# Optimization experiments

Measured on AMD Instinct MI355X. Metric: run time of the kernel, lower is better.

The kernel has to match this reference:

```python
import jax, jax.numpy as jnp
import numpy as np

EMBED_DIM = 768
NUM_HEADS = 12
HEAD_DIM = EMBED_DIM // NUM_HEADS
B, N = 4, 2048


def setup_inputs() -> dict:
    key = jax.random.key(0)
    k_x, k_wqkv, k_bqkv, k_wo, k_bo = jax.random.split(key, 5)
    s = 1.0 / np.sqrt(EMBED_DIM)
    return {
        "x": jax.random.normal(k_x, (B, N, EMBED_DIM), dtype=jnp.float32),
        # torch nn.Linear weight layout: [out_features, in_features]
        "w_qkv": jax.random.uniform(k_wqkv, (3 * EMBED_DIM, EMBED_DIM), minval=-s, maxval=s, dtype=jnp.float32),
        "b_qkv": jax.random.uniform(k_bqkv, (3 * EMBED_DIM,), minval=-s, maxval=s, dtype=jnp.float32),
        "w_out": jax.random.uniform(k_wo, (EMBED_DIM, EMBED_DIM), minval=-s, maxval=s, dtype=jnp.float32),
        "b_out": jax.random.uniform(k_bo, (EMBED_DIM,), minval=-s, maxval=s, dtype=jnp.float32),
    }


def reference(x, w_qkv, b_qkv, w_out, b_out):
    Bsz, Nlen, C = x.shape
    # fused QKV projection: [B, N, 3C]
    qkv = jnp.einsum("bnc,oc->bno", x, w_qkv) + b_qkv
    qkv = qkv.reshape(Bsz, Nlen, 3, NUM_HEADS, HEAD_DIM)
    q = qkv[:, :, 0].transpose(0, 2, 1, 3)  # [B, H, N, D]
    k = qkv[:, :, 1].transpose(0, 2, 1, 3)
    v = qkv[:, :, 2].transpose(0, 2, 1, 3)
    scale = 1.0 / np.sqrt(HEAD_DIM).astype(np.float32)
    scores = jnp.einsum("bhqd,bhkd->bhqk", q, k) * scale  # [B, H, N, N]
    attn = jax.nn.softmax(scores, axis=-1)
    ctx = jnp.einsum("bhqk,bhkd->bhqd", attn, v)  # [B, H, N, D]
    ctx = ctx.transpose(0, 2, 1, 3).reshape(Bsz, Nlen, C)
    return jnp.einsum("bnc,oc->bno", ctx, w_out) + b_out
```

## Files before the change

### kernel.cpp

```cpp
#include <hip/hip_runtime.h>
#include <math.h>

typedef __attribute__((ext_vector_type(8))) short bf16x8;
typedef __attribute__((ext_vector_type(4))) float f32x4;
typedef unsigned short u16;

namespace {
constexpr int BATCH = 4, SEQ = 2048, CDIM = 768, NH = 12, HD = 64;
constexpr int MROWS = BATCH * SEQ;
constexpr int KD = CDIM;
constexpr float QSCALE = 0.125f * 1.44269504088896f;
}

__device__ __forceinline__ u16 f2bf(float f) {
  unsigned x = __float_as_uint(f);
  return (u16)((x + 0x7fffu + ((x >> 16) & 1u)) >> 16);
}

__device__ __forceinline__ unsigned pk2bf(float a, float b) {
  unsigned r;
  asm("v_cvt_pk_bf16_f32 %0, %1, %2" : "=v"(r) : "v"(a), "v"(b));
  return r;
}

#if defined(__has_builtin)
#if __has_builtin(__builtin_amdgcn_exp2f)
#define EXP2(x) __builtin_amdgcn_exp2f(x)
#endif
#endif
#ifndef EXP2
#define EXP2(x) exp2f(x)
#endif

#define GLD16(gp, lp)                                                        \
  __builtin_amdgcn_global_load_lds(                                          \
      (const __attribute__((address_space(1))) void*)(gp),                   \
      (__attribute__((address_space(3))) void*)(lp), 16, 0, 0)

__global__ void convert_bf16(const float* __restrict__ x, u16* __restrict__ xb, int nx4,
                             const float* __restrict__ w1, u16* __restrict__ w1b, int n14,
                             const float* __restrict__ w2, u16* __restrict__ w2b, int n24) {
  const int stride = gridDim.x * blockDim.x;
  const int t0 = blockIdx.x * blockDim.x + threadIdx.x;
  for (int i = t0; i < nx4; i += stride) {
    float4 v = ((const float4*)x)[i];
    ushort4 o; o.x = f2bf(v.x); o.y = f2bf(v.y); o.z = f2bf(v.z); o.w = f2bf(v.w);
    ((ushort4*)xb)[i] = o;
  }
  for (int i = t0; i < n14; i += stride) {
    float4 v = ((const float4*)w1)[i];
    ushort4 o; o.x = f2bf(v.x); o.y = f2bf(v.y); o.z = f2bf(v.z); o.w = f2bf(v.w);
    ((ushort4*)w1b)[i] = o;
  }
  for (int i = t0; i < n24; i += stride) {
    float4 v = ((const float4*)w2)[i];
    ushort4 o; o.x = f2bf(v.x); o.y = f2bf(v.y); o.z = f2bf(v.z); o.w = f2bf(v.w);
    ((ushort4*)w2b)[i] = o;
  }
}

template <int MODE>
__global__ __launch_bounds__(512, 4) void gemm_bf16(
    const u16* __restrict__ A, const u16* __restrict__ Bw,
    const float* __restrict__ bias, float* __restrict__ outf,
    u16* __restrict__ qws, u16* __restrict__ kws, u16* __restrict__ vws) {
  __shared__ u16 smem[2 * 2 * 128 * 64];
  const int t = threadIdx.x;
  const int w = t >> 6, l = t & 63, g = l >> 4, li = l & 15;
  const int wm = w >> 1, wn = w & 1;
  const int lin = blockIdx.x;
  const int rowb = ((lin & 7) << 3) | ((lin >> 3) & 7);
  const int colb = lin >> 6;
  const int row0 = rowb * 128, col0 = colb * 128;

  const int srow = w * 16 + (l >> 3);
  const int skc = (l & 7) ^ (l >> 3);
  const u16* gA = A + (size_t)(row0 + srow) * KD + skc * 8;
  const u16* gB = Bw + (size_t)(col0 + srow) * KD + skc * 8;

  f32x4 acc[2][4];
#pragma unroll
  for (int a = 0; a < 2; ++a)
#pragma unroll
    for (int c = 0; c < 4; ++c) acc[a][c] = {0.f, 0.f, 0.f, 0.f};

#define GSTAGE(kt_, buf_)                                                     \
  do {                                                                        \
    const int k0_ = (kt_) * 64;                                               \
    u16* As_ = smem + (buf_) * (2 * 128 * 64);                                \
    u16* Bs_ = As_ + 128 * 64;                                                \
    _Pragma("unroll")                                                         \
    for (int j = 0; j < 2; ++j) {                                             \
      GLD16(gA + (size_t)8 * j * KD + k0_, &As_[(w * 16 + 8 * j) * 64]);      \
      GLD16(gB + (size_t)8 * j * KD + k0_, &Bs_[(w * 16 + 8 * j) * 64]);      \
    }                                                                         \
  } while (0)

  constexpr int NK = KD / 64;
  GSTAGE(0, 0);
  GSTAGE(1, 1);
  asm volatile("s_waitcnt vmcnt(4)" ::: "memory");
  __builtin_amdgcn_sched_barrier(0);
  __builtin_amdgcn_s_barrier();
  __builtin_amdgcn_sched_barrier(0);

  for (int kt = 0; kt < NK; ++kt) {
    const int cur = kt & 1;
    const u16* AsC = smem + cur * (2 * 128 * 64);
    const u16* BsC = AsC + 128 * 64;

    bf16x8 af[2][2], bfr[4][2];
#pragma unroll
    for (int mi = 0; mi < 2; ++mi) {
      const int r = wm * 32 + mi * 16 + li;
#pragma unroll
      for (int ks = 0; ks < 2; ++ks)
        af[mi][ks] = *(const bf16x8*)&AsC[r * 64 + (((ks * 4 + g) ^ (li & 7)) * 8)];
    }
#pragma unroll
    for (int ni = 0; ni < 4; ++ni) {
      const int r = wn * 64 + ni * 16 + li;
#pragma unroll
      for (int ks = 0; ks < 2; ++ks)
        bfr[ni][ks] = *(const bf16x8*)&BsC[r * 64 + (((ks * 4 + g) ^ (li & 7)) * 8)];
    }
    __builtin_amdgcn_s_setprio(1);
#pragma unroll
    for (int ni = 0; ni < 4; ++ni)
#pragma unroll
      for (int mi = 0; mi < 2; ++mi) {
        acc[mi][ni] = __builtin_amdgcn_mfma_f32_16x16x32_bf16(af[mi][0], bfr[ni][0], acc[mi][ni], 0, 0, 0);
        acc[mi][ni] = __builtin_amdgcn_mfma_f32_16x16x32_bf16(af[mi][1], bfr[ni][1], acc[mi][ni], 0, 0, 0);
      }
    __builtin_amdgcn_s_setprio(0);

    if (kt + 1 < NK) {
      asm volatile("s_waitcnt vmcnt(0)" ::: "memory");
      __builtin_amdgcn_sched_barrier(0);
      __builtin_amdgcn_s_barrier();
      __builtin_amdgcn_sched_barrier(0);
      if (kt + 2 < NK) GSTAGE(kt + 2, cur);
    }
  }
#undef GSTAGE

  float bsr[4];
#pragma unroll
  for (int ni = 0; ni < 4; ++ni) bsr[ni] = bias[col0 + wn * 64 + ni * 16 + li];
  const int bidx = row0 >> 11;
  const int nseq0 = row0 & (SEQ - 1);

  __syncthreads();

  if (MODE == 1) {
    float* Cf = (float*)smem;
#pragma unroll
    for (int p = 0; p < 4; ++p) {
      if (wm == p) {
#pragma unroll
        for (int mi = 0; mi < 2; ++mi)
#pragma unroll
          for (int ni = 0; ni < 4; ++ni)
#pragma unroll
            for (int i = 0; i < 4; ++i)
              Cf[(mi * 16 + 4 * g + i) * 132 + wn * 64 + ni * 16 + li] =
                  acc[mi][ni][i] + bsr[ni];
      }
      __syncthreads();
#pragma unroll
      for (int j = 0; j < 2; ++j) {
        const int fid = t + 512 * j;
        const int r = fid >> 5, c4 = (fid & 31) * 4;
        *(float4*)(outf + (size_t)(row0 + p * 32 + r) * CDIM + col0 + c4) =
            *(const float4*)&Cf[r * 132 + c4];
      }
      __syncthreads();
    }
  } else {
#pragma unroll
    for (int hc = 0; hc < 2; ++hc) {
      const int nb = col0 + hc * 64;
      const int s = nb / CDIM;
      const int h = (nb % CDIM) / HD;
      if (wn == hc) {
        if (s < 2) {
          const float qs = (s == 0) ? QSCALE : 1.f;
#pragma unroll
          for (int mi = 0; mi < 2; ++mi)
#pragma unroll
            for (int ni = 0; ni < 4; ++ni)
#pragma unroll
              for (int i = 0; i < 4; ++i)
                smem[(wm * 32 + mi * 16 + 4 * g + i) * 72 + ni * 16 + li] =
                    f2bf((acc[mi][ni][i] + bsr[ni]) * qs);
        } else {
#pragma unroll
          for (int mi = 0; mi < 2; ++mi)
#pragma unroll
            for (int ni = 0; ni < 4; ++ni)
#pragma unroll
              for (int i = 0; i < 4; ++i)
                smem[(ni * 16 + li) * 136 + wm * 32 + mi * 16 + 4 * g + i] =
                    f2bf(acc[mi][ni][i] + bsr[ni]);
        }
      }
      __syncthreads();
      if (s < 2) {
        u16* dst = (s == 0 ? qws : kws) + ((size_t)(bidx * NH + h) * SEQ + nseq0) * HD;
        const int r = t >> 3, c = (t & 7) * 8;
#pragma unroll
        for (int rd = 0; rd < 2; ++rd)
          *(uint4*)(dst + (size_t)(r + 64 * rd) * HD + c) =
              *(const uint4*)&smem[(r + 64 * rd) * 72 + c];
      } else {
        u16* dst = vws + (size_t)(bidx * NH + h) * HD * SEQ + nseq0;
        const int d = t >> 4, c = (t & 15) * 8;
#pragma unroll
        for (int rd = 0; rd < 2; ++rd)
          *(uint4*)(dst + (size_t)(d + 32 * rd) * SEQ + c) =
              *(const uint4*)&smem[(d + 32 * rd) * 136 + c];
      }
      __syncthreads();
    }
  }
}

__global__ __launch_bounds__(256, 3) void attn_mfma(
    const u16* __restrict__ qws, const u16* __restrict__ kws,
    const u16* __restrict__ vws, u16* __restrict__ ctx) {
  __shared__ u16 Ks[2][64 * 64];
  __shared__ u16 Vs[2][64 * 64];
  __shared__ u16 Ps[4 * 32 * 72];
  const int t = threadIdx.x;
  const int w = t >> 6, l = t & 63, g = l >> 4, li = l & 15;
  const int n = blockIdx.x;
  const int xcd = n & 7, j = n >> 3;
  const int hb = xcd * 6 + (j >> 4);
  const int q0 = (j & 15) * 128;
  const int h = hb % NH, b = hb / NH;
  const size_t bh = (size_t)b * NH + h;
  const u16* qb = qws + bh * SEQ * HD;
  const u16* kb = kws + bh * SEQ * HD;
  const u16* vb = vws + bh * HD * SEQ;

  bf16x8 qf[2][2];
#pragma unroll
  for (int qt = 0; qt < 2; ++qt)
#pragma unroll
    for (int ks = 0; ks < 2; ++ks)
      qf[qt][ks] = *(const bf16x8*)(qb + (size_t)(q0 + w * 32 + qt * 16 + li) * HD + ks * 32 + g * 8);
  asm volatile("s_waitcnt vmcnt(0)" ::: "memory");
  __builtin_amdgcn_sched_barrier(0);

  f32x4 acc[4][2];
#pragma unroll
  for (int dt = 0; dt < 4; ++dt)
#pragma unroll
    for (int qt = 0; qt < 2; ++qt) acc[dt][qt] = {0.f, 0.f, 0.f, 0.f};
  float lrun[2] = {0.f, 0.f};

  const int srow8 = l >> 3;
  const int skc = (l & 7) ^ srow8;
  const u16* gK = kb + (size_t)(w * 16 + srow8) * HD + skc * 8;
  const u16* gV = vb + (size_t)(w * 16 + srow8) * SEQ + skc * 8;
  u16* Pw = Ps + w * 32 * 72;

  constexpr int NT = SEQ / 64;

#define STAGE(kt_, buf_)                                                          \
  do {                                                                            \
    const int key0_ = (kt_) * 64;                                                 \
    GLD16(gK + (size_t)(key0_ + 0) * HD, &Ks[buf_][(w * 16 + 0) * 64]);           \
    GLD16(gV + (size_t)0 * SEQ + key0_, &Vs[buf_][(w * 16 + 0) * 64]);            \
    GLD16(gK + (size_t)(key0_ + 8) * HD, &Ks[buf_][(w * 16 + 8) * 64]);           \
    GLD16(gV + (size_t)8 * SEQ + key0_, &Vs[buf_][(w * 16 + 8) * 64]);            \
  } while (0)

  STAGE(0, 0);
  STAGE(1, 1);
  asm volatile("s_waitcnt vmcnt(4)" ::: "memory");
  __builtin_amdgcn_sched_barrier(0);
  __builtin_amdgcn_s_barrier();
  __builtin_amdgcn_sched_barrier(0);

  const f32x4 Z = {0.f, 0.f, 0.f, 0.f};

  for (int kt = 0; kt < NT; ++kt) {
    const int cur = kt & 1;
    const u16* KsC = Ks[cur];
    const u16* VsC = Vs[cur];

    f32x4 S[4][2];
    __builtin_amdgcn_s_setprio(1);
#pragma unroll
    for (int kb4 = 0; kb4 < 4; ++kb4) {
      bf16x8 kf0 = *(const bf16x8*)&KsC[(kb4 * 16 + li) * 64 + ((g ^ (li & 7)) * 8)];
      bf16x8 kf1 = *(const bf16x8*)&KsC[(kb4 * 16 + li) * 64 + (((4 + g) ^ (li & 7)) * 8)];
#pragma unroll
      for (int qt = 0; qt < 2; ++qt) {
        S[kb4][qt] = __builtin_amdgcn_mfma_f32_16x16x32_bf16(kf0, qf[qt][0], Z, 0, 0, 0);
        S[kb4][qt] = __builtin_amdgcn_mfma_f32_16x16x32_bf16(kf1, qf[qt][1], S[kb4][qt], 0, 0, 0);
      }
    }
    __builtin_amdgcn_s_setprio(0);

#pragma unroll
    for (int qt = 0; qt < 2; ++qt) {
      float rs = 0.f;
#pragma unroll
      for (int kb4 = 0; kb4 < 4; ++kb4) {
        const float p0 = EXP2(S[kb4][qt][0]);
        const float p1 = EXP2(S[kb4][qt][1]);
        const float p2 = EXP2(S[kb4][qt][2]);
        const float p3 = EXP2(S[kb4][qt][3]);
        rs += (p0 + p1) + (p2 + p3);
        uint2 pk;
        pk.x = pk2bf(p0, p1);
        pk.y = pk2bf(p2, p3);
        *(uint2*)&Pw[(qt * 16 + li) * 72 + ((kb4 ^ (li & 3)) * 16) + 4 * g] = pk;
      }
      lrun[qt] += rs;
    }

    bf16x8 vf[4][2];
#pragma unroll
    for (int dt = 0; dt < 4; ++dt) {
      vf[dt][0] = *(const bf16x8*)&VsC[(dt * 16 + li) * 64 + ((g ^ (li & 7)) * 8)];
      vf[dt][1] = *(const bf16x8*)&VsC[(dt * 16 + li) * 64 + (((4 + g) ^ (li & 7)) * 8)];
    }
    bf16x8 pf[2][2];
#pragma unroll
    for (int qt = 0; qt < 2; ++qt)
#pragma unroll
      for (int ks = 0; ks < 2; ++ks) {
        const int slot = (ks * 2 + (g >> 1)) ^ (li & 3);
        pf[qt][ks] = *(const bf16x8*)&Pw[(qt * 16 + li) * 72 + slot * 16 + (g & 1) * 8];
      }

    __builtin_amdgcn_s_setprio(1);
#pragma unroll
    for (int dt = 0; dt < 4; ++dt)
#pragma unroll
      for (int qt = 0; qt < 2; ++qt) {
        acc[dt][qt] = __builtin_amdgcn_mfma_f32_16x16x32_bf16(vf[dt][0], pf[qt][0], acc[dt][qt], 0, 0, 0);
        acc[dt][qt] = __builtin_amdgcn_mfma_f32_16x16x32_bf16(vf[dt][1], pf[qt][1], acc[dt][qt], 0, 0, 0);
      }
    __builtin_amdgcn_s_setprio(0);

    if (kt + 1 < NT) {
      asm volatile("s_waitcnt vmcnt(0)" ::: "memory");
      __builtin_amdgcn_sched_barrier(0);
      __builtin_amdgcn_s_barrier();
      __builtin_amdgcn_sched_barrier(0);
      if (kt + 2 < NT) STAGE(kt + 2, cur);
    }
  }
#undef STAGE

#pragma unroll
  for (int qt = 0; qt < 2; ++qt) {
    lrun[qt] += __shfl_xor(lrun[qt], 16);
    lrun[qt] += __shfl_xor(lrun[qt], 32);
  }
  float inv[2] = {1.f / lrun[0], 1.f / lrun[1]};
#pragma unroll
  for (int qt = 0; qt < 2; ++qt)
#pragma unroll
    for (int dt = 0; dt < 4; ++dt) {
      uint2 pk;
      pk.x = pk2bf(acc[dt][qt][0] * inv[qt], acc[dt][qt][1] * inv[qt]);
      pk.y = pk2bf(acc[dt][qt][2] * inv[qt], acc[dt][qt][3] * inv[qt]);
      *(uint2*)&Ps[(w * 32 + qt * 16 + li) * 72 + dt * 16 + 4 * g] = pk;
    }
  __syncthreads();
  {
    const int r = t >> 3, c = (t & 7) * 8;
#pragma unroll
    for (int rd = 0; rd < 4; ++rd)
      *(uint4*)(ctx + ((size_t)b * SEQ + q0 + r + 32 * rd) * CDIM + h * HD + c) =
          *(const uint4*)&Ps[(r + 32 * rd) * 72 + c];
  }
}

extern "C" void kernel_launch(void* const* d_in, const int* in_sizes, int n_in,
                              void* d_out, int out_size, void* d_ws, size_t ws_size,
                              hipStream_t stream) {
  (void)in_sizes; (void)n_in; (void)out_size; (void)ws_size;
  const float* x     = (const float*)d_in[0];
  const float* w_qkv = (const float*)d_in[1];
  const float* b_qkv = (const float*)d_in[2];
  const float* w_out = (const float*)d_in[3];
  const float* b_out = (const float*)d_in[4];
  float* out = (float*)d_out;

  u16* xb    = (u16*)d_ws;
  u16* wqkvb = xb + (size_t)MROWS * KD;
  u16* wob   = wqkvb + (size_t)3 * CDIM * KD;
  u16* qb    = wob + (size_t)CDIM * KD;
  const size_t QS = (size_t)BATCH * NH * SEQ * HD;
  u16* kb   = qb + QS;
  u16* vb   = kb + QS;
  u16* ctxb = vb + QS;

  hipLaunchKernelGGL(convert_bf16, dim3(2048), dim3(256), 0, stream,
                     x, xb, MROWS * KD / 4,
                     w_qkv, wqkvb, 3 * CDIM * KD / 4,
                     w_out, wob, CDIM * KD / 4);
  hipLaunchKernelGGL((gemm_bf16<0>), dim3((MROWS / 128) * (3 * CDIM / 128)), dim3(512), 0,
                     stream, xb, wqkvb, b_qkv, nullptr, qb, kb, vb);
  hipLaunchKernelGGL(attn_mfma, dim3(16 * NH * BATCH), dim3(256), 0, stream,
                     qb, kb, vb, ctxb);
  hipLaunchKernelGGL((gemm_bf16<1>), dim3((MROWS / 128) * (CDIM / 128)), dim3(512), 0,
                     stream, ctxb, wob, b_out, out, nullptr, nullptr, nullptr);
}
```

Baseline: 196.2 us.

## Rewrite attention kernel with 32x32 MFMA, register-resident P, 2-wave blocks

The attention kernel moves from 16x16x32 to 32x32x16 bf16 MFMA tiles, with each of two waves per block owning 64 query rows. The S-tile output layout is reused directly as the B operand of the PV MFMA, so the P round trip through shared memory is removed. V fragments are gathered as two 4-element halves to match that layout. The block shrinks to 128 threads, which doubles the per-wave K/V staging and raises register pressure from the 16-wide accumulators, and could cut occupancy.

```diff
diff --git a/kernel.cpp b/kernel.cpp
--- a/kernel.cpp
+++ b/kernel.cpp
@@ -2,7 +2,9 @@
 #include <math.h>
 
 typedef __attribute__((ext_vector_type(8))) short bf16x8;
+typedef __attribute__((ext_vector_type(4))) short bf16x4;
 typedef __attribute__((ext_vector_type(4))) float f32x4;
+typedef __attribute__((ext_vector_type(16))) float f32x16;
 typedef unsigned short u16;
 
 namespace {
@@ -225,127 +227,138 @@
   }
 }
 
-__global__ __launch_bounds__(256, 3) void attn_mfma(
+__global__ __launch_bounds__(128, 2) void attn_mfma(
     const u16* __restrict__ qws, const u16* __restrict__ kws,
     const u16* __restrict__ vws, u16* __restrict__ ctx) {
-  __shared__ u16 Ks[2][64 * 64];
-  __shared__ u16 Vs[2][64 * 64];
-  __shared__ u16 Ps[4 * 32 * 72];
+  __shared__ u16 smem[4 * 64 * 64];
+  u16* Ks0 = smem;
+  u16* Vs0 = smem + 2 * 64 * 64;
   const int t = threadIdx.x;
-  const int w = t >> 6, l = t & 63, g = l >> 4, li = l & 15;
+  const int w = t >> 6, l = t & 63;
+  const int hi = l >> 5, c = l & 31;
   const int n = blockIdx.x;
   const int xcd = n & 7, j = n >> 3;
   const int hb = xcd * 6 + (j >> 4);
   const int q0 = (j & 15) * 128;
   const int h = hb % NH, b = hb / NH;
   const size_t bh = (size_t)b * NH + h;
-  const u16* qb = qws + bh * SEQ * HD;
+  const u16* qbp = qws + bh * SEQ * HD;
   const u16* kb = kws + bh * SEQ * HD;
   const u16* vb = vws + bh * HD * SEQ;
-
-  bf16x8 qf[2][2];
+  const int qw = q0 + w * 64;
+
+  bf16x8 qf[2][4];
 #pragma unroll
   for (int qt = 0; qt < 2; ++qt)
 #pragma unroll
-    for (int ks = 0; ks < 2; ++ks)
-      qf[qt][ks] = *(const bf16x8*)(qb + (size_t)(q0 + w * 32 + qt * 16 + li) * HD + ks * 32 + g * 8);
+    for (int ks4 = 0; ks4 < 4; ++ks4)
+      qf[qt][ks4] = *(const bf16x8*)(qbp + (size_t)(qw + qt * 32 + c) * HD + ks4 * 16 + hi * 8);
   asm volatile("s_waitcnt vmcnt(0)" ::: "memory");
   __builtin_amdgcn_sched_barrier(0);
 
-  f32x4 acc[4][2];
-#pragma unroll
-  for (int dt = 0; dt < 4; ++dt)
-#pragma unroll
-    for (int qt = 0; qt < 2; ++qt) acc[dt][qt] = {0.f, 0.f, 0.f, 0.f};
+  f32x16 acc[2][2];
+#pragma unroll
+  for (int dt = 0; dt < 2; ++dt)
+#pragma unroll
+    for (int qt = 0; qt < 2; ++qt)
+#pragma unroll
+      for (int r = 0; r < 16; ++r) acc[dt][qt][r] = 0.f;
+  f32x16 Z;
+#pragma unroll
+  for (int r = 0; r < 16; ++r) Z[r] = 0.f;
   float lrun[2] = {0.f, 0.f};
 
   const int srow8 = l >> 3;
   const int skc = (l & 7) ^ srow8;
-  const u16* gK = kb + (size_t)(w * 16 + srow8) * HD + skc * 8;
-  const u16* gV = vb + (size_t)(w * 16 + srow8) * SEQ + skc * 8;
-  u16* Pw = Ps + w * 32 * 72;
+  const u16* gK = kb + (size_t)(w * 32 + srow8) * HD + skc * 8;
+  const u16* gV = vb + (size_t)(w * 32 + srow8) * SEQ + skc * 8;
 
   constexpr int NT = SEQ / 64;
 
-#define STAGE(kt_, buf_)                                                          \
-  do {                                                                            \
-    const int key0_ = (kt_) * 64;                                                 \
-    GLD16(gK + (size_t)(key0_ + 0) * HD, &Ks[buf_][(w * 16 + 0) * 64]);           \
-    GLD16(gV + (size_t)0 * SEQ + key0_, &Vs[buf_][(w * 16 + 0) * 64]);            \
-    GLD16(gK + (size_t)(key0_ + 8) * HD, &Ks[buf_][(w * 16 + 8) * 64]);           \
-    GLD16(gV + (size_t)8 * SEQ + key0_, &Vs[buf_][(w * 16 + 8) * 64]);            \
+#define STAGE(kt_, buf_)                                                           \
+  do {                                                                             \
+    const int key0_ = (kt_) * 64;                                                  \
+    _Pragma("unroll")                                                              \
+    for (int jj = 0; jj < 4; ++jj) {                                               \
+      GLD16(gK + (size_t)(key0_ + 8 * jj) * HD, &Ks0[(buf_) * 4096 + (w * 32 + 8 * jj) * 64]); \
+      GLD16(gV + (size_t)(8 * jj) * SEQ + key0_, &Vs0[(buf_) * 4096 + (w * 32 + 8 * jj) * 64]); \
+    }                                                                              \
   } while (0)
 
   STAGE(0, 0);
   STAGE(1, 1);
-  asm volatile("s_waitcnt vmcnt(4)" ::: "memory");
+  asm volatile("s_waitcnt vmcnt(8)" ::: "memory");
   __builtin_amdgcn_sched_barrier(0);
   __builtin_amdgcn_s_barrier();
   __builtin_amdgcn_sched_barrier(0);
-
-  const f32x4 Z = {0.f, 0.f, 0.f, 0.f};
 
   for (int kt = 0; kt < NT; ++kt) {
     const int cur = kt & 1;
-    const u16* KsC = Ks[cur];
-    const u16* VsC = Vs[cur];
-
-    f32x4 S[4][2];
-    __builtin_amdgcn_s_setprio(1);
-#pragma unroll
-    for (int kb4 = 0; kb4 < 4; ++kb4) {
-      bf16x8 kf0 = *(const bf16x8*)&KsC[(kb4 * 16 + li) * 64 + ((g ^ (li & 7)) * 8)];
-      bf16x8 kf1 = *(const bf16x8*)&KsC[(kb4 * 16 + li) * 64 + (((4 + g) ^ (li & 7)) * 8)];
+    const u16* KsC = Ks0 + cur * 4096;
+    const u16* VsC = Vs0 + cur * 4096;
+
+#pragma unroll
+    for (int kt32 = 0; kt32 < 2; ++kt32) {
+      f32x16 S0, S1;
+      __builtin_amdgcn_s_setprio(1);
+      {
+        bf16x8 kf0 = *(const bf16x8*)&KsC[(kt32 * 32 + c) * 64 + (((0 * 2 + hi) ^ (l & 7)) * 8)];
+        S0 = __builtin_amdgcn_mfma_f32_32x32x16_bf16(kf0, qf[0][0], Z, 0, 0, 0);
+        S1 = __builtin_amdgcn_mfma_f32_32x32x16_bf16(kf0, qf[1][0], Z, 0, 0, 0);
+        bf16x8 kf1 = *(const bf16x8*)&KsC[(kt32 * 32 + c) * 64 + (((1 * 2 + hi) ^ (l & 7)) * 8)];
+        S0 = __builtin_amdgcn_mfma_f32_32x32x16_bf16(kf1, qf[0][1], S0, 0, 0, 0);
+        S1 = __builtin_amdgcn_mfma_f32_32x32x16_bf16(kf1, qf[1][1], S1, 0, 0, 0);
+        bf16x8 kf2 = *(const bf16x8*)&KsC[(kt32 * 32 + c) * 64 + (((2 * 2 + hi) ^ (l & 7)) * 8)];
+        S0 = __builtin_amdgcn_mfma_f32_32x32x16_bf16(kf2, qf[0][2], S0, 0, 0, 0);
+        S1 = __builtin_amdgcn_mfma_f32_32x32x16_bf16(kf2, qf[1][2], S1, 0, 0, 0);
+        bf16x8 kf3 = *(const bf16x8*)&KsC[(kt32 * 32 + c) * 64 + (((3 * 2 + hi) ^ (l & 7)) * 8)];
+        S0 = __builtin_amdgcn_mfma_f32_32x32x16_bf16(kf3, qf[0][3], S0, 0, 0, 0);
+        S1 = __builtin_amdgcn_mfma_f32_32x32x16_bf16(kf3, qf[1][3], S1, 0, 0, 0);
+      }
+      __builtin_amdgcn_s_setprio(0);
+
+      unsigned W0[4][2], W1[4][2];
 #pragma unroll
       for (int qt = 0; qt < 2; ++qt) {
-        S[kb4][qt] = __builtin_amdgcn_mfma_f32_16x16x32_bf16(kf0, qf[qt][0], Z, 0, 0, 0);
-        S[kb4][qt] = __builtin_amdgcn_mfma_f32_16x16x32_bf16(kf1, qf[qt][1], S[kb4][qt], 0, 0, 0);
-      }
-    }
-    __builtin_amdgcn_s_setprio(0);
-
-#pragma unroll
-    for (int qt = 0; qt < 2; ++qt) {
-      float rs = 0.f;
-#pragma unroll
-      for (int kb4 = 0; kb4 < 4; ++kb4) {
-        const float p0 = EXP2(S[kb4][qt][0]);
-        const float p1 = EXP2(S[kb4][qt][1]);
-        const float p2 = EXP2(S[kb4][qt][2]);
-        const float p3 = EXP2(S[kb4][qt][3]);
-        rs += (p0 + p1) + (p2 + p3);
-        uint2 pk;
-        pk.x = pk2bf(p0, p1);
-        pk.y = pk2bf(p2, p3);
-        *(uint2*)&Pw[(qt * 16 + li) * 72 + ((kb4 ^ (li & 3)) * 16) + 4 * g] = pk;
-      }
-      lrun[qt] += rs;
-    }
-
-    bf16x8 vf[4][2];
-#pragma unroll
-    for (int dt = 0; dt < 4; ++dt) {
-      vf[dt][0] = *(const bf16x8*)&VsC[(dt * 16 + li) * 64 + ((g ^ (li & 7)) * 8)];
-      vf[dt][1] = *(const bf16x8*)&VsC[(dt * 16 + li) * 64 + (((4 + g) ^ (li & 7)) * 8)];
-    }
-    bf16x8 pf[2][2];
-#pragma unroll
-    for (int qt = 0; qt < 2; ++qt)
-#pragma unroll
-      for (int ks = 0; ks < 2; ++ks) {
-        const int slot = (ks * 2 + (g >> 1)) ^ (li & 3);
-        pf[qt][ks] = *(const bf16x8*)&Pw[(qt * 16 + li) * 72 + slot * 16 + (g & 1) * 8];
-      }
-
-    __builtin_amdgcn_s_setprio(1);
-#pragma unroll
-    for (int dt = 0; dt < 4; ++dt)
-#pragma unroll
-      for (int qt = 0; qt < 2; ++qt) {
-        acc[dt][qt] = __builtin_amdgcn_mfma_f32_16x16x32_bf16(vf[dt][0], pf[qt][0], acc[dt][qt], 0, 0, 0);
-        acc[dt][qt] = __builtin_amdgcn_mfma_f32_16x16x32_bf16(vf[dt][1], pf[qt][1], acc[dt][qt], 0, 0, 0);
-      }
-    __builtin_amdgcn_s_setprio(0);
+        const f32x16& S = (qt == 0) ? S0 : S1;
+        float rs = 0.f;
+#pragma unroll
+        for (int u = 0; u < 4; ++u) {
+          const float p0 = EXP2(S[4 * u + 0]);
+          const float p1 = EXP2(S[4 * u + 1]);
+          const float p2 = EXP2(S[4 * u + 2]);
+          const float p3 = EXP2(S[4 * u + 3]);
+          rs += (p0 + p1) + (p2 + p3);
+          unsigned lo = pk2bf(p0, p1);
+          unsigned hiw = pk2bf(p2, p3);
+          if (qt == 0) { W0[u][0] = lo; W0[u][1] = hiw; }
+          else         { W1[u][0] = lo; W1[u][1] = hiw; }
+        }
+        lrun[qt] += rs;
+      }
+
+      __builtin_amdgcn_s_setprio(1);
+#pragma unroll
+      for (int s = 0; s < 2; ++s) {
+        union { uint4 u4; bf16x8 v; } p0v, p1v;
+        p0v.u4.x = W0[2 * s][0]; p0v.u4.y = W0[2 * s][1];
+        p0v.u4.z = W0[2 * s + 1][0]; p0v.u4.w = W0[2 * s + 1][1];
+        p1v.u4.x = W1[2 * s][0]; p1v.u4.y = W1[2 * s][1];
+        p1v.u4.z = W1[2 * s + 1][0]; p1v.u4.w = W1[2 * s + 1][1];
+        const int ck0 = kt32 * 4 + 2 * s;
+        const int ck1 = ck0 + 1;
+#pragma unroll
+        for (int dt = 0; dt < 2; ++dt) {
+          const int rowoff = (dt * 32 + c) * 64;
+          union { struct { bf16x4 a, b; } p; bf16x8 v; } vfu;
+          vfu.p.a = *(const bf16x4*)&VsC[rowoff + ((ck0 ^ (l & 7)) * 8) + hi * 4];
+          vfu.p.b = *(const bf16x4*)&VsC[rowoff + ((ck1 ^ (l & 7)) * 8) + hi * 4];
+          acc[dt][0] = __builtin_amdgcn_mfma_f32_32x32x16_bf16(vfu.v, p0v.v, acc[dt][0], 0, 0, 0);
+          acc[dt][1] = __builtin_amdgcn_mfma_f32_32x32x16_bf16(vfu.v, p1v.v, acc[dt][1], 0, 0, 0);
+        }
+      }
+      __builtin_amdgcn_s_setprio(0);
+    }
 
     if (kt + 1 < NT) {
       asm volatile("s_waitcnt vmcnt(0)" ::: "memory");
@@ -357,28 +370,37 @@
   }
 #undef STAGE
 
+  float inv[2];
 #pragma unroll
   for (int qt = 0; qt < 2; ++qt) {
-    lrun[qt] += __shfl_xor(lrun[qt], 16);
     lrun[qt] += __shfl_xor(lrun[qt], 32);
-  }
-  float inv[2] = {1.f / lrun[0], 1.f / lrun[1]};
+    inv[qt] = 1.f / lrun[qt];
+  }
+  __syncthreads();
+  u16* Os = smem + w * (64 * 72);
 #pragma unroll
   for (int qt = 0; qt < 2; ++qt)
 #pragma unroll
-    for (int dt = 0; dt < 4; ++dt) {
-      uint2 pk;
-      pk.x = pk2bf(acc[dt][qt][0] * inv[qt], acc[dt][qt][1] * inv[qt]);
-      pk.y = pk2bf(acc[dt][qt][2] * inv[qt], acc[dt][qt][3] * inv[qt]);
-      *(uint2*)&Ps[(w * 32 + qt * 16 + li) * 72 + dt * 16 + 4 * g] = pk;
-    }
-  __syncthreads();
+    for (int dt = 0; dt < 2; ++dt)
+#pragma unroll
+      for (int u = 0; u < 4; ++u) {
+        uint2 pk;
+        pk.x = pk2bf(acc[dt][qt][4 * u + 0] * inv[qt], acc[dt][qt][4 * u + 1] * inv[qt]);
+        pk.y = pk2bf(acc[dt][qt][4 * u + 2] * inv[qt], acc[dt][qt][4 * u + 3] * inv[qt]);
+        const int row = qt * 32 + c;
+        const int d0 = dt * 32 + 8 * u + 4 * hi;
+        *(uint2*)&Os[row * 72 + d0] = pk;
+      }
+  asm volatile("s_waitcnt lgkmcnt(0)" ::: "memory");
+  __builtin_amdgcn_sched_barrier(0);
   {
-    const int r = t >> 3, c = (t & 7) * 8;
-#pragma unroll
-    for (int rd = 0; rd < 4; ++rd)
-      *(uint4*)(ctx + ((size_t)b * SEQ + q0 + r + 32 * rd) * CDIM + h * HD + c) =
-          *(const uint4*)&Ps[(r + 32 * rd) * 72 + c];
+    const int rr = l >> 3, cc = (l & 7) * 8;
+#pragma unroll
+    for (int it = 0; it < 8; ++it) {
+      const int row = 8 * it + rr;
+      *(uint4*)(ctx + ((size_t)b * SEQ + qw + row) * CDIM + h * HD + cc) =
+          *(const uint4*)&Os[row * 72 + cc];
+    }
   }
 }
 
@@ -408,7 +430,7 @@
                      w_out, wob, CDIM * KD / 4);
   hipLaunchKernelGGL((gemm_bf16<0>), dim3((MROWS / 128) * (3 * CDIM / 128)), dim3(512), 0,
                      stream, xb, wqkvb, b_qkv, nullptr, qb, kb, vb);
-  hipLaunchKernelGGL(attn_mfma, dim3(16 * NH * BATCH), dim3(256), 0, stream,
+  hipLaunchKernelGGL(attn_mfma, dim3(16 * NH * BATCH), dim3(128), 0, stream,
                      qb, kb, vb, ctxb);
   hipLaunchKernelGGL((gemm_bf16<1>), dim3((MROWS / 128) * (CDIM / 128)), dim3(512), 0,
                      stream, ctxb, wob, b_out, out, nullptr, nullptr, nullptr);
```

Measured after the change: 207.6 us. +5.8%, slower.

## Keep softmax probabilities in registers for PV MFMA, drop P LDS round-trip

Applied to the files above, without the earlier changes.

The PV product now feeds the bf16-packed probabilities straight from registers as the B operand, so the per-tile write of P to shared memory and its read-back are gone. The V fragments are gathered as two 4-element LDS reads, with the key ordering rearranged to match the register layout of S. The separate P buffer is removed and the epilogue reuses the K/V region behind an extra barrier, which cuts LDS use and may allow higher occupancy. The trade-off is twice as many, narrower V LDS reads and higher register pressure from holding P.

```diff
diff --git a/kernel.cpp b/kernel.cpp
--- a/kernel.cpp
+++ b/kernel.cpp
@@ -2,6 +2,7 @@
 #include <math.h>
 
 typedef __attribute__((ext_vector_type(8))) short bf16x8;
+typedef __attribute__((ext_vector_type(4))) short bf16x4;
 typedef __attribute__((ext_vector_type(4))) float f32x4;
 typedef unsigned short u16;
 
@@ -228,9 +229,9 @@
 __global__ __launch_bounds__(256, 3) void attn_mfma(
     const u16* __restrict__ qws, const u16* __restrict__ kws,
     const u16* __restrict__ vws, u16* __restrict__ ctx) {
-  __shared__ u16 Ks[2][64 * 64];
-  __shared__ u16 Vs[2][64 * 64];
-  __shared__ u16 Ps[4 * 32 * 72];
+  __shared__ u16 smem[4 * 64 * 64 + 256];
+  u16* Ks0 = smem;
+  u16* Vs0 = smem + 2 * 64 * 64;
   const int t = threadIdx.x;
   const int w = t >> 6, l = t & 63, g = l >> 4, li = l & 15;
   const int n = blockIdx.x;
@@ -239,7 +240,7 @@
   const int q0 = (j & 15) * 128;
   const int h = hb % NH, b = hb / NH;
   const size_t bh = (size_t)b * NH + h;
-  const u16* qb = qws + bh * SEQ * HD;
+  const u16* qbp = qws + bh * SEQ * HD;
   const u16* kb = kws + bh * SEQ * HD;
   const u16* vb = vws + bh * HD * SEQ;
 
@@ -248,7 +249,7 @@
   for (int qt = 0; qt < 2; ++qt)
 #pragma unroll
     for (int ks = 0; ks < 2; ++ks)
-      qf[qt][ks] = *(const bf16x8*)(qb + (size_t)(q0 + w * 32 + qt * 16 + li) * HD + ks * 32 + g * 8);
+      qf[qt][ks] = *(const bf16x8*)(qbp + (size_t)(q0 + w * 32 + qt * 16 + li) * HD + ks * 32 + g * 8);
   asm volatile("s_waitcnt vmcnt(0)" ::: "memory");
   __builtin_amdgcn_sched_barrier(0);
 
@@ -263,17 +264,16 @@
   const int skc = (l & 7) ^ srow8;
   const u16* gK = kb + (size_t)(w * 16 + srow8) * HD + skc * 8;
   const u16* gV = vb + (size_t)(w * 16 + srow8) * SEQ + skc * 8;
-  u16* Pw = Ps + w * 32 * 72;
 
   constexpr int NT = SEQ / 64;
 
 #define STAGE(kt_, buf_)                                                          \
   do {                                                                            \
     const int key0_ = (kt_) * 64;                                                 \
-    GLD16(gK + (size_t)(key0_ + 0) * HD, &Ks[buf_][(w * 16 + 0) * 64]);           \
-    GLD16(gV + (size_t)0 * SEQ + key0_, &Vs[buf_][(w * 16 + 0) * 64]);            \
-    GLD16(gK + (size_t)(key0_ + 8) * HD, &Ks[buf_][(w * 16 + 8) * 64]);           \
-    GLD16(gV + (size_t)8 * SEQ + key0_, &Vs[buf_][(w * 16 + 8) * 64]);            \
+    GLD16(gK + (size_t)(key0_ + 0) * HD, &Ks0[(buf_) * 4096 + (w * 16 + 0) * 64]); \
+    GLD16(gV + (size_t)0 * SEQ + key0_, &Vs0[(buf_) * 4096 + (w * 16 + 0) * 64]); \
+    GLD16(gK + (size_t)(key0_ + 8) * HD, &Ks0[(buf_) * 4096 + (w * 16 + 8) * 64]); \
+    GLD16(gV + (size_t)8 * SEQ + key0_, &Vs0[(buf_) * 4096 + (w * 16 + 8) * 64]); \
   } while (0)
 
   STAGE(0, 0);
@@ -287,8 +287,8 @@
 
   for (int kt = 0; kt < NT; ++kt) {
     const int cur = kt & 1;
-    const u16* KsC = Ks[cur];
-    const u16* VsC = Vs[cur];
+    const u16* KsC = Ks0 + cur * 4096;
+    const u16* VsC = Vs0 + cur * 4096;
 
     f32x4 S[4][2];
     __builtin_amdgcn_s_setprio(1);
@@ -304,6 +304,7 @@
     }
     __builtin_amdgcn_s_setprio(0);
 
+    unsigned W[2][4][2];
 #pragma unroll
     for (int qt = 0; qt < 2; ++qt) {
       float rs = 0.f;
@@ -314,37 +315,33 @@
         const float p2 = EXP2(S[kb4][qt][2]);
         const float p3 = EXP2(S[kb4][qt][3]);
         rs += (p0 + p1) + (p2 + p3);
-        uint2 pk;
-        pk.x = pk2bf(p0, p1);
-        pk.y = pk2bf(p2, p3);
-        *(uint2*)&Pw[(qt * 16 + li) * 72 + ((kb4 ^ (li & 3)) * 16) + 4 * g] = pk;
+        W[qt][kb4][0] = pk2bf(p0, p1);
+        W[qt][kb4][1] = pk2bf(p2, p3);
       }
       lrun[qt] += rs;
     }
 
-    bf16x8 vf[4][2];
-#pragma unroll
-    for (int dt = 0; dt < 4; ++dt) {
-      vf[dt][0] = *(const bf16x8*)&VsC[(dt * 16 + li) * 64 + ((g ^ (li & 7)) * 8)];
-      vf[dt][1] = *(const bf16x8*)&VsC[(dt * 16 + li) * 64 + (((4 + g) ^ (li & 7)) * 8)];
-    }
-    bf16x8 pf[2][2];
-#pragma unroll
-    for (int qt = 0; qt < 2; ++qt)
-#pragma unroll
-      for (int ks = 0; ks < 2; ++ks) {
-        const int slot = (ks * 2 + (g >> 1)) ^ (li & 3);
-        pf[qt][ks] = *(const bf16x8*)&Pw[(qt * 16 + li) * 72 + slot * 16 + (g & 1) * 8];
-      }
-
     __builtin_amdgcn_s_setprio(1);
 #pragma unroll
-    for (int dt = 0; dt < 4; ++dt)
-#pragma unroll
-      for (int qt = 0; qt < 2; ++qt) {
-        acc[dt][qt] = __builtin_amdgcn_mfma_f32_16x16x32_bf16(vf[dt][0], pf[qt][0], acc[dt][qt], 0, 0, 0);
-        acc[dt][qt] = __builtin_amdgcn_mfma_f32_16x16x32_bf16(vf[dt][1], pf[qt][1], acc[dt][qt], 0, 0, 0);
-      }
+    for (int ks = 0; ks < 2; ++ks) {
+      union { uint4 u4; bf16x8 v; } pf0, pf1;
+      pf0.u4.x = W[0][2 * ks][0];     pf0.u4.y = W[0][2 * ks][1];
+      pf0.u4.z = W[0][2 * ks + 1][0]; pf0.u4.w = W[0][2 * ks + 1][1];
+      pf1.u4.x = W[1][2 * ks][0];     pf1.u4.y = W[1][2 * ks][1];
+      pf1.u4.z = W[1][2 * ks + 1][0]; pf1.u4.w = W[1][2 * ks + 1][1];
+#pragma unroll
+      for (int dt = 0; dt < 4; ++dt) {
+        const int d = dt * 16 + li;
+        const int base = d * 64 + (g & 1) * 4;
+        const int s0 = ((ks * 4 + (g >> 1)) ^ (d & 7)) * 8;
+        const int s1 = ((ks * 4 + 2 + (g >> 1)) ^ (d & 7)) * 8;
+        union { struct { bf16x4 a, b; } p; bf16x8 v; } vfu;
+        vfu.p.a = *(const bf16x4*)&VsC[base + s0];
+        vfu.p.b = *(const bf16x4*)&VsC[base + s1];
+        acc[dt][0] = __builtin_amdgcn_mfma_f32_16x16x32_bf16(vfu.v, pf0.v, acc[dt][0], 0, 0, 0);
+        acc[dt][1] = __builtin_amdgcn_mfma_f32_16x16x32_bf16(vfu.v, pf1.v, acc[dt][1], 0, 0, 0);
+      }
+    }
     __builtin_amdgcn_s_setprio(0);
 
     if (kt + 1 < NT) {
@@ -363,6 +360,7 @@
     lrun[qt] += __shfl_xor(lrun[qt], 32);
   }
   float inv[2] = {1.f / lrun[0], 1.f / lrun[1]};
+  __syncthreads();
 #pragma unroll
   for (int qt = 0; qt < 2; ++qt)
 #pragma unroll
@@ -370,7 +368,7 @@
       uint2 pk;
       pk.x = pk2bf(acc[dt][qt][0] * inv[qt], acc[dt][qt][1] * inv[qt]);
       pk.y = pk2bf(acc[dt][qt][2] * inv[qt], acc[dt][qt][3] * inv[qt]);
-      *(uint2*)&Ps[(w * 32 + qt * 16 + li) * 72 + dt * 16 + 4 * g] = pk;
+      *(uint2*)&smem[(w * 32 + qt * 16 + li) * 72 + dt * 16 + 4 * g] = pk;
     }
   __syncthreads();
   {
@@ -378,7 +376,7 @@
 #pragma unroll
     for (int rd = 0; rd < 4; ++rd)
       *(uint4*)(ctx + ((size_t)b * SEQ + q0 + r + 32 * rd) * CDIM + h * HD + c) =
-          *(const uint4*)&Ps[(r + 32 * rd) * 72 + c];
+          *(const uint4*)&smem[(r + 32 * rd) * 72 + c];
   }
 }
 
```

Result: no change. 197.1 us (median of 2 runs) (+0.5%).
